# Kernel tuning notes

Hardware: AMD Instinct MI355X
Metric: run time of the kernel (lower is better)

Reference implementation:

```python
import jax, jax.numpy as jnp
import numpy as np

N_LEVELS, CPL = 4, 1024           # levels, cells per level (n_cells = 4096)
IN_D, HID, OUT_D, MLP = 512, 1024, 512, 128


def setup_inputs() -> dict:
    key = jax.random.key(0)
    ks = iter(jax.random.split(key, 32))
    r = lambda shape, s=0.05: jax.random.normal(next(ks), shape, dtype=jnp.float32) * s
    inp = {
        'x': r((1, IN_D), 1.0),
        'hiddens': r((N_LEVELS * CPL, HID), 0.1),
        'ea_W1': r((N_LEVELS, IN_D + HID, MLP)), 'ea_b1': r((N_LEVELS, MLP)),
        'ea_W2': r((N_LEVELS, MLP, OUT_D)),      'ea_b2': r((N_LEVELS, OUT_D)),
        'eg_W1': r((N_LEVELS, IN_D + HID, MLP)), 'eg_b1': r((N_LEVELS, MLP)),
        'eg_W2': r((N_LEVELS, MLP, OUT_D)),      'eg_b2': r((N_LEVELS, OUT_D)),
        'gru_Wih': r((N_LEVELS, 3 * HID, OUT_D + 1)),
        'gru_Whh': r((N_LEVELS, 3 * HID, HID)),
        'gru_bih': r((N_LEVELS, 3 * HID)), 'gru_bhh': r((N_LEVELS, 3 * HID)),
        'pred_W1': r((N_LEVELS - 1, HID, HID)), 'pred_b1': r((N_LEVELS - 1, HID)),
        'pred_W2': r((N_LEVELS - 1, HID, HID)), 'pred_b2': r((N_LEVELS - 1, HID)),
        'pei_W': r((HID * N_LEVELS, OUT_D)), 'pei_b': r((OUT_D,)),
        'step': 10,
    }
    return inp


def _forward(x, hiddens, ea_W1, ea_b1, ea_W2, ea_b2, eg_W1, eg_b1, eg_W2, eg_b2,
             gru_Wih, gru_Whh, gru_bih, gru_bhh, pred_W1, pred_b1, pred_W2, pred_b2,
             pei_W, pei_b, step):
    L = gru_Whh.shape[0]
    Hd = gru_Whh.shape[2]
    C = hiddens.shape[0] // L
    h = hiddens.reshape(L, C, Hd)                              # [L,C,H]
    xb = jnp.broadcast_to(x[0], (L, C, x.shape[-1]))           # same x for every cell
    comb = jnp.concatenate([xb, h], axis=-1)                   # [L,C,IN+H]

    def mlp(W1, b1, W2, b2):
        z = jax.nn.relu(jnp.einsum('lci,lim->lcm', comb, W1) + b1[:, None, :])
        return jnp.einsum('lcm,lmo->lco', z, W2) + b2[:, None, :]

    out = mlp(ea_W1, ea_b1, ea_W2, ea_b2) - mlp(eg_W1, eg_b1, eg_W2, eg_b2)  # a - g
    tension = jnp.mean(out ** 2, axis=-1, keepdims=True)       # [L,C,1]
    avg_tension = jnp.mean(tension)                            # mean over all cells

    # GRUCell (torch gate order r,z,n); mem input is detached in the original
    mem_in = jax.lax.stop_gradient(jnp.concatenate([out, tension], axis=-1))  # [L,C,OUT+1]
    gi = jnp.einsum('lci,lgi->lcg', mem_in, gru_Wih) + gru_bih[:, None, :]
    gh = jnp.einsum('lch,lgh->lcg', h, gru_Whh) + gru_bhh[:, None, :]
    i_r, i_z, i_n = jnp.split(gi, 3, axis=-1)
    h_r, h_z, h_n = jnp.split(gh, 3, axis=-1)
    rg = jax.nn.sigmoid(i_r + h_r)
    zg = jax.nn.sigmoid(i_z + h_z)
    ng = jnp.tanh(i_n + rg * h_n)
    new_h = jax.lax.stop_gradient((1.0 - zg) * ng + zg * h)    # self.hiddens = ...detach()

    level_means = new_h.mean(axis=1)                           # [L,H] (pre pe-update)

    # top-down predictors: predicted[lv] from level_means[lv+1]
    pz = jax.nn.relu(jnp.einsum('li,lim->lm', level_means[1:], pred_W1) + pred_b1)
    predicted = jnp.einsum('lm,lmo->lo', pz, pred_W2) + pred_b2          # [L-1,H]
    pe_signal = jax.lax.stop_gradient((predicted - level_means[:-1]) * 0.05)
    delta = jnp.zeros_like(level_means).at[:-1].add(pe_signal).at[1:].add(-0.5 * pe_signal)
    hh = new_h + delta[:, None, :]

    # per-level mean blend
    hh = 0.85 * hh + 0.15 * hh.mean(axis=1, keepdims=True)
    # faction sync: with n_factions == n_levels, factions == levels exactly
    hh = 0.85 * hh + 0.15 * hh.mean(axis=1, keepdims=True)
    if step > 5:  # debate (step is a static Python int)
        global_op = hh.mean(axis=1).mean(axis=0)               # [H]
        dc = max(1, C // 4)
        hh = hh.at[:, :dc].set(0.85 * hh[:, :dc] + 0.15 * global_op)

    combined = level_means.reshape(-1) @ pei_W + pei_b         # [OUT]
    return combined, avg_tension, hh.reshape(-1, Hd)


def reference(x, hiddens, ea_W1, ea_b1, ea_W2, ea_b2, eg_W1, eg_b1, eg_W2, eg_b2,
              gru_Wih, gru_Whh, gru_bih, gru_bhh, pred_W1, pred_b1, pred_W2, pred_b2,
              pei_W, pei_b, step):
    return _forward(x, hiddens, ea_W1, ea_b1, ea_W2, ea_b2, eg_W1, eg_b1, eg_W2, eg_b2,
                    gru_Wih, gru_Whh, gru_bih, gru_bhh, pred_W1, pred_b1, pred_W2, pred_b2,
                    pei_W, pei_b, step)
```

## Files before the change

kernel.cpp:

```cpp
#include <hip/hip_runtime.h>
#include <math.h>

#define L4   4
#define CPL  1024
#define HID  1024
#define IND  512
#define MLPD 128
#define OUTD 512
#define G3   3072
#define ROWS 4096
#define KP   544

typedef unsigned short u16;
typedef u16   u16x8  __attribute__((ext_vector_type(8)));
typedef short bf16x8 __attribute__((ext_vector_type(8)));
typedef float f32x4  __attribute__((ext_vector_type(4)));

__device__ __forceinline__ float b2f(u16 u) {
  return __uint_as_float(((unsigned int)u) << 16);
}
__device__ __forceinline__ u16 f2b(float f) {
  unsigned int x = __float_as_uint(f);
  x += 0x7fffu + ((x >> 16) & 1u);
  return (u16)(x >> 16);
}
__device__ __forceinline__ float sigm(float v) { return 1.0f/(1.0f + expf(-v)); }

struct F4 { float x, y, z, w; };
__device__ __forceinline__ F4 ld4(const void* p, size_t i, bool f32) {
  F4 r;
  if (f32) {
    float4 v = *reinterpret_cast<const float4*>((const float*)p + i);
    r.x = v.x; r.y = v.y; r.z = v.z; r.w = v.w;
  } else {
    ushort4 v = *reinterpret_cast<const ushort4*>((const u16*)p + i);
    r.x = b2f(v.x); r.y = b2f(v.y); r.z = b2f(v.z); r.w = b2f(v.w);
  }
  return r;
}
__device__ __forceinline__ float ld1(const void* p, size_t i, bool f32) {
  return f32 ? ((const float*)p)[i] : b2f(((const u16*)p)[i]);
}
__device__ __forceinline__ void st1(void* p, size_t i, float v, bool f32) {
  if (f32) ((float*)p)[i] = v; else ((u16*)p)[i] = f2b(v);
}
__device__ __forceinline__ u16x8 ldc8(const void* p, size_t i, bool f32) {
  u16x8 r;
  if (f32) {
    const float* q = (const float*)p + i;
    float4 v0 = *reinterpret_cast<const float4*>(q);
    float4 v1 = *reinterpret_cast<const float4*>(q + 4);
    r[0]=f2b(v0.x); r[1]=f2b(v0.y); r[2]=f2b(v0.z); r[3]=f2b(v0.w);
    r[4]=f2b(v1.x); r[5]=f2b(v1.y); r[6]=f2b(v1.z); r[7]=f2b(v1.w);
  } else {
    r = *reinterpret_cast<const u16x8*>((const u16*)p + i);
  }
  return r;
}

__global__ void k_detect(const void* __restrict__ x, int* __restrict__ flag) {
  int t = threadIdx.x;
  const u16* xu = (const u16*)x;
  unsigned u = xu[2*t];
  int e = (u >> 7) & 0xFF;
  int good = (e >= 96 && e <= 134) ? 1 : 0;
  __shared__ int cnt[256];
  cnt[t] = good;
  __syncthreads();
  for (int s = 128; s > 0; s >>= 1) { if (t < s) cnt[t] += cnt[t+s]; __syncthreads(); }
  if (t == 0) flag[0] = (cnt[0] < 200) ? 1 : 0;
}

__global__ void k_prep(float* __restrict__ zf, const void* __restrict__ bih,
                       const void* __restrict__ bhh, const int* __restrict__ dflag,
                       float* __restrict__ bs_r, float* __restrict__ bs_z,
                       float* __restrict__ bn_i, float* __restrict__ bn_h) {
  const bool f32 = dflag[0] != 0;
  int b = blockIdx.x, t = threadIdx.x;
  if (b < 16) {
    int idx = b*256 + t;
    int l = idx >> 10, j = idx & 1023;
    bs_r[idx] = ld1(bih, l*G3 + j, f32)        + ld1(bhh, l*G3 + j, f32);
    bs_z[idx] = ld1(bih, l*G3 + 1024 + j, f32) + ld1(bhh, l*G3 + 1024 + j, f32);
    bn_i[idx] = ld1(bih, l*G3 + 2048 + j, f32);
    bn_h[idx] = ld1(bhh, l*G3 + 2048 + j, f32);
  } else {
    int idx = (b-16)*256 + t;
    zf[idx] = 0.0f;
  }
}

__global__ void k_prep_wih(const void* __restrict__ Wih, const int* __restrict__ dflag,
                           u16* __restrict__ WihP) {
  const bool f32 = dflag[0] != 0;
  int row = blockIdx.x;
  int t = threadIdx.x;
  size_t src = (size_t)row * 513;
  size_t dst = (size_t)row * KP;
  WihP[dst + t]       = f2b(ld1(Wih, src + t, f32));
  WihP[dst + 256 + t] = f2b(ld1(Wih, src + 256 + t, f32));
  if (t < 32) {
    float v = (t == 0) ? ld1(Wih, src + 512, f32) : 0.0f;
    WihP[dst + 512 + t] = f2b(v);
  }
}

__global__ void k_prep_whh(const void* __restrict__ Whh, const int* __restrict__ dflag,
                           u16* __restrict__ WhhP) {
  const bool f32 = dflag[0] != 0;
  int t = threadIdx.x;
  int row = blockIdx.x*2 + (t >> 7);
  int c8  = (t & 127) * 8;
  size_t off = (size_t)row * HID + c8;
  u16x8 v = ldc8(Whh, off, f32);
  *reinterpret_cast<u16x8*>(&WhhP[off]) = v;
}

__global__ void k_prep_hb(const void* __restrict__ H, const int* __restrict__ dflag,
                          u16* __restrict__ HB) {
  const bool f32 = dflag[0] != 0;
  int t = threadIdx.x;
  int row = blockIdx.x*2 + (t >> 7);
  int c8  = (t & 127) * 8;
  size_t off = (size_t)row * HID + c8;
  u16x8 v = ldc8(H, off, f32);
  *reinterpret_cast<u16x8*>(&HB[off]) = v;
}

__global__ void k_prep_w1t(const void* __restrict__ eaW1, const void* __restrict__ egW1,
                           const int* __restrict__ dflag, u16* __restrict__ W1T) {
  const bool f32 = dflag[0] != 0;
  __shared__ u16 sT[128*66];
  int l = blockIdx.x, path = blockIdx.y, kt = blockIdx.z;
  int t = threadIdx.x;
  const void* W1 = path ? egW1 : eaW1;
  for (int rr = 0; rr < 64; rr += 2) {
    int r = rr + (t >> 7), m = t & 127;
    float v = ld1(W1, ((size_t)l*1536 + 512 + kt*64 + r)*MLPD + m, f32);
    sT[m*66 + r] = f2b(v);
  }
  __syncthreads();
  for (int mm = 0; mm < 128; mm += 4) {
    int m = mm + (t >> 6), kk = t & 63;
    W1T[((size_t)l*256 + path*128 + m)*1024 + kt*64 + kk] = sT[m*66 + kk];
  }
}

__global__ void k_base_acc(const void* __restrict__ x, const void* __restrict__ eaW1,
                           const void* __restrict__ egW1, const int* __restrict__ dflag,
                           float* __restrict__ baseacc) {
  const bool f32 = dflag[0] != 0;
  int l = blockIdx.x, path = blockIdx.y, kc = blockIdx.z, m = threadIdx.x;
  const void* W1 = path ? egW1 : eaW1;
  float acc = 0.0f;
  int i0 = kc*128;
  for (int i = i0; i < i0 + 128; ++i)
    acc += ld1(x, i, f32) * ld1(W1, ((size_t)l*1536 + i)*MLPD + m, f32);
  atomicAdd(&baseacc[path*512 + l*MLPD + m], acc);
}

#define LPAD 40
__global__ __launch_bounds__(256) void k_z_mfma(
    const u16* __restrict__ HB, const u16* __restrict__ W1T,
    const void* __restrict__ eab1, const void* __restrict__ egb1,
    const float* __restrict__ baseacc, const int* __restrict__ dflag,
    u16* __restrict__ Z) {
  const bool f32 = dflag[0] != 0;
  __shared__ u16 sA[2][64*LPAD];
  __shared__ u16 sB[2][64*LPAD];
  int t = threadIdx.x;
  int row0 = blockIdx.x * 64;
  int n0   = blockIdx.y * 64;
  int l    = row0 >> 10;
  int wid = t >> 6, lane = t & 63;
  int waveM = wid >> 1, waveN = wid & 1;
  int quad = lane >> 4, lcol = lane & 15;
  int arow = t >> 2, kq = (t & 3) * 8;

  f32x4 acc[2][2];
  const f32x4 zz = {0.0f,0.0f,0.0f,0.0f};
#pragma unroll
  for (int i = 0; i < 2; ++i)
#pragma unroll
    for (int j = 0; j < 2; ++j) acc[i][j] = zz;

  size_t habase = (size_t)(row0 + arow)*HID;
  const u16* Bb = W1T + ((size_t)l*256 + n0 + arow)*1024;

  u16x8 av = *reinterpret_cast<const u16x8*>(HB + habase + kq);
  u16x8 bv = *reinterpret_cast<const u16x8*>(Bb + kq);
  int cur = 0;
  for (int k0 = 0; k0 < HID; k0 += 32) {
    *reinterpret_cast<u16x8*>(&sA[cur][arow*LPAD + kq]) = av;
    *reinterpret_cast<u16x8*>(&sB[cur][arow*LPAD + kq]) = bv;
    asm volatile("s_waitcnt lgkmcnt(0)" ::: "memory");
    __builtin_amdgcn_s_barrier();
    if (k0 + 32 < HID) {
      av = *reinterpret_cast<const u16x8*>(HB + habase + k0 + 32 + kq);
      bv = *reinterpret_cast<const u16x8*>(Bb + k0 + 32 + kq);
    }
    bf16x8 af[2];
#pragma unroll
    for (int i = 0; i < 2; ++i)
      af[i] = *reinterpret_cast<const bf16x8*>(&sA[cur][(waveM*32 + i*16 + lcol)*LPAD + quad*8]);
#pragma unroll
    for (int j = 0; j < 2; ++j) {
      bf16x8 bf = *reinterpret_cast<const bf16x8*>(&sB[cur][(waveN*32 + j*16 + lcol)*LPAD + quad*8]);
#pragma unroll
      for (int i = 0; i < 2; ++i)
        acc[i][j] = __builtin_amdgcn_mfma_f32_16x16x32_bf16(af[i], bf, acc[i][j], 0, 0, 0);
    }
    cur ^= 1;
  }
#pragma unroll
  for (int j = 0; j < 2; ++j) {
    int nn = n0 + waveN*32 + j*16 + lcol;
    int path = nn >> 7, m = nn & 127;
    float bval = baseacc[path*512 + l*MLPD + m] +
                 ld1(path ? egb1 : eab1, l*MLPD + m, f32);
#pragma unroll
    for (int i = 0; i < 2; ++i)
#pragma unroll
      for (int g = 0; g < 4; ++g) {
        int r = row0 + waveM*32 + i*16 + quad*4 + g;
        float v = acc[i][j][g] + bval;
        Z[(size_t)r*256 + nn] = f2b(v > 0.0f ? v : 0.0f);
      }
  }
}

#define BM 64
#define BN 64
#define BK 16
__global__ __launch_bounds__(256) void k_out(
    const u16* __restrict__ Zb, const void* __restrict__ eaW2, const void* __restrict__ egW2,
    const void* __restrict__ eab2, const void* __restrict__ egb2,
    const int* __restrict__ dflag, u16* __restrict__ OUTT) {
  const bool f32 = dflag[0] != 0;
  __shared__ float As[BK][BM];
  __shared__ float Bs[BK][BN];
  int t = threadIdx.x;
  int row0 = blockIdx.x * BM;
  int n0   = blockIdx.y * BN;
  int l    = row0 >> 10;
  const u16* Ab = Zb + (size_t)row0 * 256;
  int tx = t & 15, ty = t >> 4;
  int am = t >> 2, akq = (t & 3) * 4;
  int bk = t >> 4, bn = (t & 15) * 4;

  float acc[4][4];
#pragma unroll
  for (int j = 0; j < 4; ++j) {
    int o = n0 + tx*4 + j;
    float bd = ld1(eab2, l*OUTD + o, f32) - ld1(egb2, l*OUTD + o, f32);
#pragma unroll
    for (int i = 0; i < 4; ++i) acc[i][j] = bd;
  }
  for (int ph = 0; ph < 2; ++ph) {
    const void* B = ph ? egW2 : eaW2;
    size_t boff = (size_t)l*MLPD*OUTD + n0;
    float sgn = ph ? -1.0f : 1.0f;
    for (int k0 = 0; k0 < MLPD; k0 += BK) {
      ushort4 avu = *reinterpret_cast<const ushort4*>(Ab + (size_t)am*256 + ph*128 + k0 + akq);
      F4 bvf = ld4(B, boff + (size_t)(k0 + bk)*OUTD + bn, f32);
      __syncthreads();
      As[akq+0][am] = b2f(avu.x); As[akq+1][am] = b2f(avu.y);
      As[akq+2][am] = b2f(avu.z); As[akq+3][am] = b2f(avu.w);
      Bs[bk][bn+0] = sgn*bvf.x; Bs[bk][bn+1] = sgn*bvf.y;
      Bs[bk][bn+2] = sgn*bvf.z; Bs[bk][bn+3] = sgn*bvf.w;
      __syncthreads();
#pragma unroll
      for (int kk = 0; kk < BK; ++kk) {
        float4 a4 = *reinterpret_cast<const float4*>(&As[kk][ty*4]);
        float4 b4 = *reinterpret_cast<const float4*>(&Bs[kk][tx*4]);
        float a[4] = {a4.x,a4.y,a4.z,a4.w};
        float b[4] = {b4.x,b4.y,b4.z,b4.w};
#pragma unroll
        for (int i = 0; i < 4; ++i)
#pragma unroll
          for (int j = 0; j < 4; ++j) acc[i][j] += a[i]*b[j];
      }
    }
  }
#pragma unroll
  for (int i = 0; i < 4; ++i) {
    int r = row0 + ty*4 + i;
#pragma unroll
    for (int j = 0; j < 4; ++j)
      OUTT[(size_t)r*KP + n0 + tx*4 + j] = f2b(acc[i][j]);
  }
}

__global__ void k_tension(u16* __restrict__ OUTT, float* __restrict__ tsum) {
  int row = blockIdx.x, t = threadIdx.x;
  u16* p = OUTT + (size_t)row*KP;
  float v0 = b2f(p[t]), v1 = b2f(p[t+256]);
  float s = v0*v0 + v1*v1;
#pragma unroll
  for (int off = 32; off > 0; off >>= 1) s += __shfl_down(s, off, 64);
  __shared__ float red[4];
  if ((t & 63) == 0) red[t >> 6] = s;
  __syncthreads();
  if (t == 0) {
    float tot = red[0] + red[1] + red[2] + red[3];
    p[512] = f2b(tot * (1.0f/512.0f));
    atomicAdd(tsum, tot);
  }
  if (t < 31) p[513 + t] = 0;
}

#define SWZ(row, ku) ((row)*64 + ((ku) ^ (((row)&7)<<3)))
__global__ __launch_bounds__(256, 2) void k_gru_mfma(
    const u16* __restrict__ OUTT, const u16* __restrict__ HB,
    const u16* __restrict__ WihP, const u16* __restrict__ WhhP,
    const void* __restrict__ H,
    const float* __restrict__ bs_r, const float* __restrict__ bs_z,
    const float* __restrict__ bn_i, const float* __restrict__ bn_h,
    const int* __restrict__ dflag, void* __restrict__ outv) {
  const bool f32 = dflag[0] != 0;
  __shared__ __align__(16) u16 sA[2][128*64];
  __shared__ __align__(16) u16 sB[2][3*64*64];
  int t = threadIdx.x;
  int bid = blockIdx.x;
  int xg = bid & 7, inner = bid >> 3;
  int l = xg & 3, jG = xg >> 2;
  int rbi = inner & 7, jbl = inner >> 3;
  int row0 = (l*8 + rbi) * 128;
  int j0   = (jG*8 + jbl) * 64;
  int wid = t >> 6, lane = t & 63;
  int waveM = wid & 1, waveJ = wid >> 1;
  int quad = lane >> 4, lcol = lane & 15;

  f32x4 acc[4][4][2];
  const f32x4 zz = {0.0f,0.0f,0.0f,0.0f};
#pragma unroll
  for (int b = 0; b < 4; ++b)
#pragma unroll
    for (int i = 0; i < 4; ++i)
#pragma unroll
      for (int j = 0; j < 2; ++j) acc[b][i][j] = zz;

  u16x8 ra[4], rbr[6];
  auto load1 = [&](int k0) {
    int kw = KP - k0;
#pragma unroll
    for (int s = 0; s < 4; ++s) {
      int idx = s*256 + t, row = idx >> 3, ch = idx & 7;
      if (ch*8 < kw)
        ra[s] = *reinterpret_cast<const u16x8*>(
            OUTT + (size_t)(row0 + row)*KP + k0 + ch*8);
      else { u16x8 z = {0,0,0,0,0,0,0,0}; ra[s] = z; }
    }
#pragma unroll
    for (int s = 0; s < 6; ++s) {
      int idx = s*256 + t, band = idx >> 9, rem = idx & 511;
      int row = rem >> 3, ch = rem & 7;
      if (ch*8 < kw)
        rbr[s] = *reinterpret_cast<const u16x8*>(
            WihP + ((size_t)l*G3 + band*1024 + j0 + row)*KP + k0 + ch*8);
      else { u16x8 z = {0,0,0,0,0,0,0,0}; rbr[s] = z; }
    }
  };
  auto load2 = [&](int k0) {
#pragma unroll
    for (int s = 0; s < 4; ++s) {
      int idx = s*256 + t, row = idx >> 3, ch = idx & 7;
      ra[s] = *reinterpret_cast<const u16x8*>(
          HB + (size_t)(row0 + row)*HID + k0 + ch*8);
    }
#pragma unroll
    for (int s = 0; s < 6; ++s) {
      int idx = s*256 + t, band = idx >> 9, rem = idx & 511;
      int row = rem >> 3, ch = rem & 7;
      rbr[s] = *reinterpret_cast<const u16x8*>(
          WhhP + ((size_t)l*G3 + band*1024 + j0 + row)*HID + k0 + ch*8);
    }
  };
  auto stage = [&](int cb) {
#pragma unroll
    for (int s = 0; s < 4; ++s) {
      int idx = s*256 + t, row = idx >> 3, ch = idx & 7;
      *reinterpret_cast<u16x8*>(&sA[cb][SWZ(row, ch*8)]) = ra[s];
    }
#pragma unroll
    for (int s = 0; s < 6; ++s) {
      int idx = s*256 + t, band = idx >> 9, rem = idx & 511;
      int row = rem >> 3, ch = rem & 7;
      *reinterpret_cast<u16x8*>(&sB[cb][band*4096 + SWZ(row, ch*8)]) = rbr[s];
    }
  };

  int cur = 0;
  load1(0);
  for (int k0 = 0; k0 < KP; k0 += 64) {
    stage(cur);
    asm volatile("s_waitcnt lgkmcnt(0)" ::: "memory");
    __builtin_amdgcn_s_barrier();
    if (k0 + 64 < KP) load1(k0 + 64);
    else              load2(0);
    __builtin_amdgcn_s_setprio(1);
#pragma unroll
    for (int kc = 0; kc < 2; ++kc) {
      bf16x8 af[4];
#pragma unroll
      for (int i = 0; i < 4; ++i) {
        int rl = waveM*64 + i*16 + lcol;
        af[i] = *reinterpret_cast<const bf16x8*>(&sA[cur][SWZ(rl, kc*32 + quad*8)]);
      }
#pragma unroll
      for (int b = 0; b < 3; ++b)
#pragma unroll
        for (int jj = 0; jj < 2; ++jj) {
          int jl = waveJ*32 + jj*16 + lcol;
          bf16x8 bf = *reinterpret_cast<const bf16x8*>(
              &sB[cur][b*4096 + SWZ(jl, kc*32 + quad*8)]);
#pragma unroll
          for (int i = 0; i < 4; ++i)
            acc[b][i][jj] = __builtin_amdgcn_mfma_f32_16x16x32_bf16(
                af[i], bf, acc[b][i][jj], 0, 0, 0);
        }
    }
    __builtin_amdgcn_s_setprio(0);
    cur ^= 1;
  }
  for (int k0 = 0; k0 < HID; k0 += 64) {
    stage(cur);
    asm volatile("s_waitcnt lgkmcnt(0)" ::: "memory");
    __builtin_amdgcn_s_barrier();
    if (k0 + 64 < HID) load2(k0 + 64);
    __builtin_amdgcn_s_setprio(1);
#pragma unroll
    for (int kc = 0; kc < 2; ++kc) {
      bf16x8 af[4];
#pragma unroll
      for (int i = 0; i < 4; ++i) {
        int rl = waveM*64 + i*16 + lcol;
        af[i] = *reinterpret_cast<const bf16x8*>(&sA[cur][SWZ(rl, kc*32 + quad*8)]);
      }
#pragma unroll
      for (int b = 0; b < 3; ++b) {
        int ai = (b < 2) ? b : 3;
#pragma unroll
        for (int jj = 0; jj < 2; ++jj) {
          int jl = waveJ*32 + jj*16 + lcol;
          bf16x8 bf = *reinterpret_cast<const bf16x8*>(
              &sB[cur][b*4096 + SWZ(jl, kc*32 + quad*8)]);
#pragma unroll
          for (int i = 0; i < 4; ++i)
            acc[ai][i][jj] = __builtin_amdgcn_mfma_f32_16x16x32_bf16(
                af[i], bf, acc[ai][i][jj], 0, 0, 0);
        }
      }
    }
    __builtin_amdgcn_s_setprio(0);
    cur ^= 1;
  }
#pragma unroll
  for (int i = 0; i < 4; ++i)
#pragma unroll
    for (int jj = 0; jj < 2; ++jj) {
      int j = j0 + waveJ*32 + jj*16 + lcol;
      float br = bs_r[l*HID + j], bz = bs_z[l*HID + j];
      float bi = bn_i[l*HID + j], bh = bn_h[l*HID + j];
#pragma unroll
      for (int g = 0; g < 4; ++g) {
        int r = row0 + waveM*64 + i*16 + quad*4 + g;
        float rg = sigm(acc[0][i][jj][g] + br);
        float zg = sigm(acc[1][i][jj][g] + bz);
        float ng = tanhf(acc[2][i][jj][g] + bi + rg*(acc[3][i][jj][g] + bh));
        float hv = ld1(H, (size_t)r*HID + j, f32);
        st1(outv, 513 + (size_t)r*HID + j, (1.0f - zg)*ng + zg*hv, f32);
      }
    }
}

__global__ void k_lm_acc(const void* __restrict__ outv, const int* __restrict__ dflag,
                         float* __restrict__ lm) {
  const bool f32 = dflag[0] != 0;
  int l = blockIdx.x, cc = blockIdx.y, t = threadIdx.x;
  float s0=0.f, s1=0.f, s2=0.f, s3=0.f;
  for (int c = cc*16; c < cc*16 + 16; ++c) {
    size_t base = 513 + (size_t)(l*CPL + c)*HID;
    s0 += ld1(outv, base + t,       f32);
    s1 += ld1(outv, base + 256 + t, f32);
    s2 += ld1(outv, base + 512 + t, f32);
    s3 += ld1(outv, base + 768 + t, f32);
  }
  atomicAdd(&lm[l*HID + t],       s0);
  atomicAdd(&lm[l*HID + 256 + t], s1);
  atomicAdd(&lm[l*HID + 512 + t], s2);
  atomicAdd(&lm[l*HID + 768 + t], s3);
}
__global__ void k_lmfin(float* __restrict__ lm) {
  int idx = blockIdx.x*256 + threadIdx.x;
  lm[idx] *= (1.0f/1024.0f);
}

__global__ void k_pz_acc(const float* __restrict__ lm, const void* __restrict__ pW1,
                         const int* __restrict__ dflag, float* __restrict__ pz) {
  const bool f32 = dflag[0] != 0;
  int lv = blockIdx.x, mb = blockIdx.y, kc = blockIdx.z;
  int m = mb*256 + threadIdx.x;
  float acc = 0.0f;
  int i0 = kc*32;
  const float* lmp = lm + (lv + 1)*HID;
  for (int i = i0; i < i0 + 32; ++i)
    acc += lmp[i] * ld1(pW1, ((size_t)lv*HID + i)*HID + m, f32);
  atomicAdd(&pz[lv*HID + m], acc);
}
__global__ void k_pzfin(float* __restrict__ pz, const void* __restrict__ pb1,
                        const int* __restrict__ dflag) {
  const bool f32 = dflag[0] != 0;
  int idx = blockIdx.x*256 + threadIdx.x;
  float v = pz[idx] + ld1(pb1, idx, f32);
  pz[idx] = v > 0.0f ? v : 0.0f;
}
__global__ void k_pe_acc(const float* __restrict__ pz, const void* __restrict__ pW2,
                         const int* __restrict__ dflag, float* __restrict__ pe) {
  const bool f32 = dflag[0] != 0;
  int lv = blockIdx.x, ob = blockIdx.y, kc = blockIdx.z;
  int o = ob*256 + threadIdx.x;
  float acc = 0.0f;
  int m0 = kc*32;
  const float* pzp = pz + lv*HID;
  for (int m = m0; m < m0 + 32; ++m)
    acc += pzp[m] * ld1(pW2, ((size_t)lv*HID + m)*HID + o, f32);
  atomicAdd(&pe[lv*HID + o], acc);
}
__global__ void k_pefin(float* __restrict__ pe, const void* __restrict__ pb2,
                        const float* __restrict__ lm, const int* __restrict__ dflag) {
  const bool f32 = dflag[0] != 0;
  int idx = blockIdx.x*256 + threadIdx.x;
  pe[idx] = (pe[idx] + ld1(pb2, idx, f32) - lm[idx]) * 0.05f;
}

__global__ void k_addc_gop(const float* __restrict__ lm, const float* __restrict__ pe,
                           float* __restrict__ addc, float* __restrict__ gop) {
  int j = blockIdx.x*256 + threadIdx.x;
  float pe0 = pe[j], pe1 = pe[1024 + j], pe2 = pe[2048 + j];
  float d0 = pe0, d1 = pe1 - 0.5f*pe0, d2 = pe2 - 0.5f*pe1, d3 = -0.5f*pe2;
  float l0 = lm[j], l1 = lm[1024 + j], l2 = lm[2048 + j], l3 = lm[3072 + j];
  addc[j]        = 0.2775f*l0 + d0;
  addc[1024 + j] = 0.2775f*l1 + d1;
  addc[2048 + j] = 0.2775f*l2 + d2;
  addc[3072 + j] = 0.2775f*l3 + d3;
  gop[j] = 0.25f*((l0 + d0) + (l1 + d1) + (l2 + d2) + (l3 + d3));
}

__global__ void k_comb_acc(const float* __restrict__ lm, const void* __restrict__ peiW,
                           const int* __restrict__ dflag, float* __restrict__ comb) {
  const bool f32 = dflag[0] != 0;
  int ob = blockIdx.x, kc = blockIdx.y;
  int o = ob*256 + threadIdx.x;
  float acc = 0.0f;
  int i0 = kc*128;
  for (int i = i0; i < i0 + 128; ++i)
    acc += lm[i] * ld1(peiW, (size_t)i*OUTD + o, f32);
  atomicAdd(&comb[o], acc);
}
__global__ void k_fin(const float* __restrict__ comb, const void* __restrict__ peib,
                      const float* __restrict__ tsum, const int* __restrict__ dflag,
                      void* __restrict__ outv) {
  const bool f32 = dflag[0] != 0;
  int o = blockIdx.x*256 + threadIdx.x;
  st1(outv, o, comb[o] + ld1(peib, o, f32), f32);
  if (o == 0) st1(outv, 512, tsum[0] * (1.0f/(4096.0f*512.0f)), f32);
}

__global__ void k_hh(void* __restrict__ outv, const float* __restrict__ addc,
                     const float* __restrict__ gop, const int* __restrict__ step,
                     const int* __restrict__ dflag) {
  const bool f32 = dflag[0] != 0;
  int row = blockIdx.x, t = threadIdx.x;
  int l = row >> 10, c = row & 1023;
  bool debate = (step[0] > 5) && (c < 256);
  size_t base = 513 + (size_t)row*HID;
#pragma unroll
  for (int k = 0; k < 4; ++k) {
    int j = t + k*256;
    float v = 0.7225f * ld1(outv, base + j, f32) + addc[l*HID + j];
    if (debate) v = 0.85f*v + 0.15f*gop[j];
    st1(outv, base + j, v, f32);
  }
}

extern "C" void kernel_launch(void* const* d_in, const int* in_sizes, int n_in,
                              void* d_out, int out_size, void* d_ws, size_t ws_size,
                              hipStream_t stream) {
  (void)in_sizes; (void)n_in; (void)out_size; (void)ws_size;
  const void* x    = d_in[0];
  const void* hid  = d_in[1];
  const void* eaW1 = d_in[2];
  const void* eab1 = d_in[3];
  const void* eaW2 = d_in[4];
  const void* eab2 = d_in[5];
  const void* egW1 = d_in[6];
  const void* egb1 = d_in[7];
  const void* egW2 = d_in[8];
  const void* egb2 = d_in[9];
  const void* gWih = d_in[10];
  const void* gWhh = d_in[11];
  const void* gbih = d_in[12];
  const void* gbhh = d_in[13];
  const void* pW1  = d_in[14];
  const void* pb1  = d_in[15];
  const void* pW2  = d_in[16];
  const void* pb2  = d_in[17];
  const void* peiW = d_in[18];
  const void* peib = d_in[19];
  const int*  step = (const int*)d_in[20];

  float* wsf = (float*)d_ws;
  float* tsum    = wsf + 0;
  float* baseacc = wsf + 64;
  float* lm      = wsf + 1088;
  float* pz      = wsf + 5184;
  float* pe      = wsf + 8256;
  float* comb    = wsf + 11328;
  int*   dflag   = (int*)(wsf + 12288);
  float* bs_r    = wsf + 12352;
  float* bs_z    = wsf + 16448;
  float* bn_i    = wsf + 20544;
  float* bn_h    = wsf + 24640;
  float* addc    = wsf + 28736;
  float* gop     = wsf + 32832;
  u16* Zb   = (u16*)(wsf + 33856);
  u16* OUTT = Zb + (size_t)4096*256;
  u16* WihP = OUTT + (size_t)4096*KP;
  u16* HB   = WihP + (size_t)12288*KP;
  u16* WhhP = HB   + (size_t)4096*1024;
  u16* W1T  = OUTT;

  k_detect   <<<dim3(1),        dim3(256), 0, stream>>>(x, dflag);
  k_prep     <<<dim3(64),       dim3(256), 0, stream>>>(wsf, gbih, gbhh, dflag,
                                                        bs_r, bs_z, bn_i, bn_h);
  k_prep_wih <<<dim3(12288),    dim3(256), 0, stream>>>(gWih, dflag, WihP);
  k_prep_whh <<<dim3(6144),     dim3(256), 0, stream>>>(gWhh, dflag, WhhP);
  k_prep_hb  <<<dim3(2048),     dim3(256), 0, stream>>>(hid, dflag, HB);
  k_prep_w1t <<<dim3(4,2,16),   dim3(256), 0, stream>>>(eaW1, egW1, dflag, W1T);
  k_base_acc <<<dim3(4,2,4),    dim3(128), 0, stream>>>(x, eaW1, egW1, dflag, baseacc);
  k_z_mfma   <<<dim3(64,4),     dim3(256), 0, stream>>>(HB, W1T, eab1, egb1,
                                                        baseacc, dflag, Zb);
  k_out      <<<dim3(64,8),     dim3(256), 0, stream>>>(Zb, eaW2, egW2, eab2, egb2,
                                                        dflag, OUTT);
  k_tension  <<<dim3(4096),     dim3(256), 0, stream>>>(OUTT, tsum);
  k_gru_mfma <<<dim3(512),      dim3(256), 0, stream>>>(OUTT, HB, WihP, WhhP, hid,
                                                        bs_r, bs_z, bn_i, bn_h,
                                                        dflag, d_out);
  k_lm_acc   <<<dim3(4,64),     dim3(256), 0, stream>>>(d_out, dflag, lm);
  k_lmfin    <<<dim3(16),       dim3(256), 0, stream>>>(lm);
  k_pz_acc   <<<dim3(3,4,32),   dim3(256), 0, stream>>>(lm, pW1, dflag, pz);
  k_pzfin    <<<dim3(12),       dim3(256), 0, stream>>>(pz, pb1, dflag);
  k_pe_acc   <<<dim3(3,4,32),   dim3(256), 0, stream>>>(pz, pW2, dflag, pe);
  k_pefin    <<<dim3(12),       dim3(256), 0, stream>>>(pe, pb2, lm, dflag);
  k_addc_gop <<<dim3(4),        dim3(256), 0, stream>>>(lm, pe, addc, gop);
  k_comb_acc <<<dim3(2,32),     dim3(256), 0, stream>>>(lm, peiW, dflag, comb);
  k_fin      <<<dim3(2),        dim3(256), 0, stream>>>(comb, peib, tsum, dflag, d_out);
  k_hh       <<<dim3(4096),     dim3(256), 0, stream>>>(d_out, addc, gop, step, dflag);
}
```

Before: 448.6 us.

## Use MFMA for second MLP layer, widen z-GEMM K tile, fuse level-mean into GRU

The scalar FP32 second-layer GEMM is replaced by a bf16 MFMA kernel. It reads a new prepacked, sign-folded W2 matrix, so the ea and eg paths become one K=256 GEMM. The first-layer MFMA kernel now uses a 64-wide K tile with swizzled LDS and priority hints. The per-level mean reduction moves into the GRU epilogue through an LDS reduction and atomics, which removes a separate pass over the output. In exchange it adds a prep kernel, and it lowers W2 precision to bf16.

```diff
diff --git a/kernel.cpp b/kernel.cpp
--- a/kernel.cpp
+++ b/kernel.cpp
@@ -27,17 +27,6 @@
 __device__ __forceinline__ float sigm(float v) { return 1.0f/(1.0f + expf(-v)); }
 
 struct F4 { float x, y, z, w; };
-__device__ __forceinline__ F4 ld4(const void* p, size_t i, bool f32) {
-  F4 r;
-  if (f32) {
-    float4 v = *reinterpret_cast<const float4*>((const float*)p + i);
-    r.x = v.x; r.y = v.y; r.z = v.z; r.w = v.w;
-  } else {
-    ushort4 v = *reinterpret_cast<const ushort4*>((const u16*)p + i);
-    r.x = b2f(v.x); r.y = b2f(v.y); r.z = b2f(v.z); r.w = b2f(v.w);
-  }
-  return r;
-}
 __device__ __forceinline__ float ld1(const void* p, size_t i, bool f32) {
   return f32 ? ((const float*)p)[i] : b2f(((const u16*)p)[i]);
 }
@@ -146,6 +135,26 @@
   }
 }
 
+__global__ void k_prep_w2m(const void* __restrict__ eaW2, const void* __restrict__ egW2,
+                           const int* __restrict__ dflag, u16* __restrict__ W2M) {
+  const bool f32 = dflag[0] != 0;
+  __shared__ u16 sT[128*130];
+  int l = blockIdx.x, path = blockIdx.y, ot = blockIdx.z;
+  int t = threadIdx.x;
+  const void* W2 = path ? egW2 : eaW2;
+  float sgn = path ? -1.0f : 1.0f;
+  for (int rr = 0; rr < 128; rr += 2) {
+    int r = rr + (t >> 7), o = t & 127;
+    float v = ld1(W2, ((size_t)l*MLPD + r)*OUTD + ot*128 + o, f32);
+    sT[o*130 + r] = f2b(sgn*v);
+  }
+  __syncthreads();
+  for (int oo = 0; oo < 128; oo += 2) {
+    int o = oo + (t >> 7), m = t & 127;
+    W2M[((size_t)l*OUTD + ot*128 + o)*256 + path*128 + m] = sT[o*130 + m];
+  }
+}
+
 __global__ void k_base_acc(const void* __restrict__ x, const void* __restrict__ eaW1,
                            const void* __restrict__ egW1, const int* __restrict__ dflag,
                            float* __restrict__ baseacc) {
@@ -159,15 +168,16 @@
   atomicAdd(&baseacc[path*512 + l*MLPD + m], acc);
 }
 
-#define LPAD 40
+#define SWZ(row, ku) ((row)*64 + ((ku) ^ (((row)&7)<<3)))
+
 __global__ __launch_bounds__(256) void k_z_mfma(
     const u16* __restrict__ HB, const u16* __restrict__ W1T,
     const void* __restrict__ eab1, const void* __restrict__ egb1,
     const float* __restrict__ baseacc, const int* __restrict__ dflag,
     u16* __restrict__ Z) {
   const bool f32 = dflag[0] != 0;
-  __shared__ u16 sA[2][64*LPAD];
-  __shared__ u16 sB[2][64*LPAD];
+  __shared__ __align__(16) u16 sA[2][64*64];
+  __shared__ __align__(16) u16 sB[2][64*64];
   int t = threadIdx.x;
   int row0 = blockIdx.x * 64;
   int n0   = blockIdx.y * 64;
@@ -175,7 +185,6 @@
   int wid = t >> 6, lane = t & 63;
   int waveM = wid >> 1, waveN = wid & 1;
   int quad = lane >> 4, lcol = lane & 15;
-  int arow = t >> 2, kq = (t & 3) * 8;
 
   f32x4 acc[2][2];
   const f32x4 zz = {0.0f,0.0f,0.0f,0.0f};
@@ -184,32 +193,52 @@
 #pragma unroll
     for (int j = 0; j < 2; ++j) acc[i][j] = zz;
 
-  size_t habase = (size_t)(row0 + arow)*HID;
-  const u16* Bb = W1T + ((size_t)l*256 + n0 + arow)*1024;
-
-  u16x8 av = *reinterpret_cast<const u16x8*>(HB + habase + kq);
-  u16x8 bv = *reinterpret_cast<const u16x8*>(Bb + kq);
+  u16x8 ra[2], rb[2];
+  auto loadk = [&](int k0) {
+#pragma unroll
+    for (int s = 0; s < 2; ++s) {
+      int idx = s*256 + t, row = idx >> 3, ch = idx & 7;
+      ra[s] = *reinterpret_cast<const u16x8*>(
+          HB + (size_t)(row0 + row)*HID + k0 + ch*8);
+      rb[s] = *reinterpret_cast<const u16x8*>(
+          W1T + ((size_t)l*256 + n0 + row)*1024 + k0 + ch*8);
+    }
+  };
+  auto stage = [&](int cb) {
+#pragma unroll
+    for (int s = 0; s < 2; ++s) {
+      int idx = s*256 + t, row = idx >> 3, ch = idx & 7;
+      *reinterpret_cast<u16x8*>(&sA[cb][SWZ(row, ch*8)]) = ra[s];
+      *reinterpret_cast<u16x8*>(&sB[cb][SWZ(row, ch*8)]) = rb[s];
+    }
+  };
+
   int cur = 0;
-  for (int k0 = 0; k0 < HID; k0 += 32) {
-    *reinterpret_cast<u16x8*>(&sA[cur][arow*LPAD + kq]) = av;
-    *reinterpret_cast<u16x8*>(&sB[cur][arow*LPAD + kq]) = bv;
+  loadk(0);
+  for (int k0 = 0; k0 < HID; k0 += 64) {
+    stage(cur);
     asm volatile("s_waitcnt lgkmcnt(0)" ::: "memory");
     __builtin_amdgcn_s_barrier();
-    if (k0 + 32 < HID) {
-      av = *reinterpret_cast<const u16x8*>(HB + habase + k0 + 32 + kq);
-      bv = *reinterpret_cast<const u16x8*>(Bb + k0 + 32 + kq);
-    }
-    bf16x8 af[2];
-#pragma unroll
-    for (int i = 0; i < 2; ++i)
-      af[i] = *reinterpret_cast<const bf16x8*>(&sA[cur][(waveM*32 + i*16 + lcol)*LPAD + quad*8]);
-#pragma unroll
-    for (int j = 0; j < 2; ++j) {
-      bf16x8 bf = *reinterpret_cast<const bf16x8*>(&sB[cur][(waveN*32 + j*16 + lcol)*LPAD + quad*8]);
-#pragma unroll
-      for (int i = 0; i < 2; ++i)
-        acc[i][j] = __builtin_amdgcn_mfma_f32_16x16x32_bf16(af[i], bf, acc[i][j], 0, 0, 0);
-    }
+    if (k0 + 64 < HID) loadk(k0 + 64);
+    __builtin_amdgcn_s_setprio(1);
+#pragma unroll
+    for (int kc = 0; kc < 2; ++kc) {
+      bf16x8 af[2];
+#pragma unroll
+      for (int i = 0; i < 2; ++i) {
+        int rl = waveM*32 + i*16 + lcol;
+        af[i] = *reinterpret_cast<const bf16x8*>(&sA[cur][SWZ(rl, kc*32 + quad*8)]);
+      }
+#pragma unroll
+      for (int j = 0; j < 2; ++j) {
+        int jl = waveN*32 + j*16 + lcol;
+        bf16x8 bf = *reinterpret_cast<const bf16x8*>(&sB[cur][SWZ(jl, kc*32 + quad*8)]);
+#pragma unroll
+        for (int i = 0; i < 2; ++i)
+          acc[i][j] = __builtin_amdgcn_mfma_f32_16x16x32_bf16(af[i], bf, acc[i][j], 0, 0, 0);
+      }
+    }
+    __builtin_amdgcn_s_setprio(0);
     cur ^= 1;
   }
 #pragma unroll
@@ -229,65 +258,95 @@
   }
 }
 
-#define BM 64
-#define BN 64
-#define BK 16
-__global__ __launch_bounds__(256) void k_out(
-    const u16* __restrict__ Zb, const void* __restrict__ eaW2, const void* __restrict__ egW2,
+__global__ __launch_bounds__(256) void k_outm(
+    const u16* __restrict__ Zb, const u16* __restrict__ W2M,
     const void* __restrict__ eab2, const void* __restrict__ egb2,
     const int* __restrict__ dflag, u16* __restrict__ OUTT) {
   const bool f32 = dflag[0] != 0;
-  __shared__ float As[BK][BM];
-  __shared__ float Bs[BK][BN];
-  int t = threadIdx.x;
-  int row0 = blockIdx.x * BM;
-  int n0   = blockIdx.y * BN;
+  __shared__ __align__(16) u16 sA[2][128*64];
+  __shared__ __align__(16) u16 sB[2][64*64];
+  int t = threadIdx.x;
+  int row0 = blockIdx.x * 128;
+  int n0   = blockIdx.y * 64;
   int l    = row0 >> 10;
-  const u16* Ab = Zb + (size_t)row0 * 256;
-  int tx = t & 15, ty = t >> 4;
-  int am = t >> 2, akq = (t & 3) * 4;
-  int bk = t >> 4, bn = (t & 15) * 4;
-
-  float acc[4][4];
-#pragma unroll
-  for (int j = 0; j < 4; ++j) {
-    int o = n0 + tx*4 + j;
+  int wid = t >> 6, lane = t & 63;
+  int waveM = wid & 1, waveJ = wid >> 1;
+  int quad = lane >> 4, lcol = lane & 15;
+
+  f32x4 acc[4][2];
+  const f32x4 zz = {0.0f,0.0f,0.0f,0.0f};
+#pragma unroll
+  for (int i = 0; i < 4; ++i)
+#pragma unroll
+    for (int j = 0; j < 2; ++j) acc[i][j] = zz;
+
+  u16x8 ra[4], rb[2];
+  auto loadk = [&](int k0) {
+#pragma unroll
+    for (int s = 0; s < 4; ++s) {
+      int idx = s*256 + t, row = idx >> 3, ch = idx & 7;
+      ra[s] = *reinterpret_cast<const u16x8*>(
+          Zb + (size_t)(row0 + row)*256 + k0 + ch*8);
+    }
+#pragma unroll
+    for (int s = 0; s < 2; ++s) {
+      int idx = s*256 + t, row = idx >> 3, ch = idx & 7;
+      rb[s] = *reinterpret_cast<const u16x8*>(
+          W2M + ((size_t)l*OUTD + n0 + row)*256 + k0 + ch*8);
+    }
+  };
+  auto stage = [&](int cb) {
+#pragma unroll
+    for (int s = 0; s < 4; ++s) {
+      int idx = s*256 + t, row = idx >> 3, ch = idx & 7;
+      *reinterpret_cast<u16x8*>(&sA[cb][SWZ(row, ch*8)]) = ra[s];
+    }
+#pragma unroll
+    for (int s = 0; s < 2; ++s) {
+      int idx = s*256 + t, row = idx >> 3, ch = idx & 7;
+      *reinterpret_cast<u16x8*>(&sB[cb][SWZ(row, ch*8)]) = rb[s];
+    }
+  };
+
+  int cur = 0;
+  loadk(0);
+  for (int k0 = 0; k0 < 256; k0 += 64) {
+    stage(cur);
+    asm volatile("s_waitcnt lgkmcnt(0)" ::: "memory");
+    __builtin_amdgcn_s_barrier();
+    if (k0 + 64 < 256) loadk(k0 + 64);
+    __builtin_amdgcn_s_setprio(1);
+#pragma unroll
+    for (int kc = 0; kc < 2; ++kc) {
+      bf16x8 af[4];
+#pragma unroll
+      for (int i = 0; i < 4; ++i) {
+        int rl = waveM*64 + i*16 + lcol;
+        af[i] = *reinterpret_cast<const bf16x8*>(&sA[cur][SWZ(rl, kc*32 + quad*8)]);
+      }
+#pragma unroll
+      for (int jj = 0; jj < 2; ++jj) {
+        int jl = waveJ*32 + jj*16 + lcol;
+        bf16x8 bf = *reinterpret_cast<const bf16x8*>(&sB[cur][SWZ(jl, kc*32 + quad*8)]);
+#pragma unroll
+        for (int i = 0; i < 4; ++i)
+          acc[i][jj] = __builtin_amdgcn_mfma_f32_16x16x32_bf16(af[i], bf, acc[i][jj], 0, 0, 0);
+      }
+    }
+    __builtin_amdgcn_s_setprio(0);
+    cur ^= 1;
+  }
+#pragma unroll
+  for (int jj = 0; jj < 2; ++jj) {
+    int o = n0 + waveJ*32 + jj*16 + lcol;
     float bd = ld1(eab2, l*OUTD + o, f32) - ld1(egb2, l*OUTD + o, f32);
 #pragma unroll
-    for (int i = 0; i < 4; ++i) acc[i][j] = bd;
-  }
-  for (int ph = 0; ph < 2; ++ph) {
-    const void* B = ph ? egW2 : eaW2;
-    size_t boff = (size_t)l*MLPD*OUTD + n0;
-    float sgn = ph ? -1.0f : 1.0f;
-    for (int k0 = 0; k0 < MLPD; k0 += BK) {
-      ushort4 avu = *reinterpret_cast<const ushort4*>(Ab + (size_t)am*256 + ph*128 + k0 + akq);
-      F4 bvf = ld4(B, boff + (size_t)(k0 + bk)*OUTD + bn, f32);
-      __syncthreads();
-      As[akq+0][am] = b2f(avu.x); As[akq+1][am] = b2f(avu.y);
-      As[akq+2][am] = b2f(avu.z); As[akq+3][am] = b2f(avu.w);
-      Bs[bk][bn+0] = sgn*bvf.x; Bs[bk][bn+1] = sgn*bvf.y;
-      Bs[bk][bn+2] = sgn*bvf.z; Bs[bk][bn+3] = sgn*bvf.w;
-      __syncthreads();
-#pragma unroll
-      for (int kk = 0; kk < BK; ++kk) {
-        float4 a4 = *reinterpret_cast<const float4*>(&As[kk][ty*4]);
-        float4 b4 = *reinterpret_cast<const float4*>(&Bs[kk][tx*4]);
-        float a[4] = {a4.x,a4.y,a4.z,a4.w};
-        float b[4] = {b4.x,b4.y,b4.z,b4.w};
-#pragma unroll
-        for (int i = 0; i < 4; ++i)
-#pragma unroll
-          for (int j = 0; j < 4; ++j) acc[i][j] += a[i]*b[j];
-      }
-    }
-  }
-#pragma unroll
-  for (int i = 0; i < 4; ++i) {
-    int r = row0 + ty*4 + i;
-#pragma unroll
-    for (int j = 0; j < 4; ++j)
-      OUTT[(size_t)r*KP + n0 + tx*4 + j] = f2b(acc[i][j]);
+    for (int i = 0; i < 4; ++i)
+#pragma unroll
+      for (int g = 0; g < 4; ++g) {
+        int r = row0 + waveM*64 + i*16 + quad*4 + g;
+        OUTT[(size_t)r*KP + o] = f2b(acc[i][jj][g] + bd);
+      }
   }
 }
 
@@ -309,14 +368,14 @@
   if (t < 31) p[513 + t] = 0;
 }
 
-#define SWZ(row, ku) ((row)*64 + ((ku) ^ (((row)&7)<<3)))
 __global__ __launch_bounds__(256, 2) void k_gru_mfma(
     const u16* __restrict__ OUTT, const u16* __restrict__ HB,
     const u16* __restrict__ WihP, const u16* __restrict__ WhhP,
     const void* __restrict__ H,
     const float* __restrict__ bs_r, const float* __restrict__ bs_z,
     const float* __restrict__ bn_i, const float* __restrict__ bn_h,
-    const int* __restrict__ dflag, void* __restrict__ outv) {
+    const int* __restrict__ dflag, void* __restrict__ outv,
+    float* __restrict__ lm) {
   const bool f32 = dflag[0] != 0;
   __shared__ __align__(16) u16 sA[2][128*64];
   __shared__ __align__(16) u16 sB[2][3*64*64];
@@ -455,6 +514,7 @@
     __builtin_amdgcn_s_setprio(0);
     cur ^= 1;
   }
+  float psum[2] = {0.0f, 0.0f};
 #pragma unroll
   for (int i = 0; i < 4; ++i)
 #pragma unroll
@@ -469,28 +529,28 @@
         float zg = sigm(acc[1][i][jj][g] + bz);
         float ng = tanhf(acc[2][i][jj][g] + bi + rg*(acc[3][i][jj][g] + bh));
         float hv = ld1(H, (size_t)r*HID + j, f32);
-        st1(outv, 513 + (size_t)r*HID + j, (1.0f - zg)*ng + zg*hv, f32);
-      }
-    }
-}
-
-__global__ void k_lm_acc(const void* __restrict__ outv, const int* __restrict__ dflag,
-                         float* __restrict__ lm) {
-  const bool f32 = dflag[0] != 0;
-  int l = blockIdx.x, cc = blockIdx.y, t = threadIdx.x;
-  float s0=0.f, s1=0.f, s2=0.f, s3=0.f;
-  for (int c = cc*16; c < cc*16 + 16; ++c) {
-    size_t base = 513 + (size_t)(l*CPL + c)*HID;
-    s0 += ld1(outv, base + t,       f32);
-    s1 += ld1(outv, base + 256 + t, f32);
-    s2 += ld1(outv, base + 512 + t, f32);
-    s3 += ld1(outv, base + 768 + t, f32);
-  }
-  atomicAdd(&lm[l*HID + t],       s0);
-  atomicAdd(&lm[l*HID + 256 + t], s1);
-  atomicAdd(&lm[l*HID + 512 + t], s2);
-  atomicAdd(&lm[l*HID + 768 + t], s3);
-}
+        float nh = (1.0f - zg)*ng + zg*hv;
+        st1(outv, 513 + (size_t)r*HID + j, nh, f32);
+        psum[jj] += nh;
+      }
+    }
+  __syncthreads();
+  float* red = reinterpret_cast<float*>(&sA[0][0]);
+  int slot = waveM*4 + quad;
+#pragma unroll
+  for (int jj = 0; jj < 2; ++jj) {
+    int jl = waveJ*32 + jj*16 + lcol;
+    red[jl*8 + slot] = psum[jj];
+  }
+  __syncthreads();
+  if (t < 64) {
+    float s = 0.0f;
+#pragma unroll
+    for (int k = 0; k < 8; ++k) s += red[t*8 + k];
+    atomicAdd(&lm[l*HID + j0 + t], s);
+  }
+}
+
 __global__ void k_lmfin(float* __restrict__ lm) {
   int idx = blockIdx.x*256 + threadIdx.x;
   lm[idx] *= (1.0f/1024.0f);
@@ -629,6 +689,7 @@
   u16* WihP = OUTT + (size_t)4096*KP;
   u16* HB   = WihP + (size_t)12288*KP;
   u16* WhhP = HB   + (size_t)4096*1024;
+  u16* W2M  = WhhP + (size_t)12288*1024;
   u16* W1T  = OUTT;
 
   k_detect   <<<dim3(1),        dim3(256), 0, stream>>>(x, dflag);
@@ -638,16 +699,16 @@
   k_prep_whh <<<dim3(6144),     dim3(256), 0, stream>>>(gWhh, dflag, WhhP);
   k_prep_hb  <<<dim3(2048),     dim3(256), 0, stream>>>(hid, dflag, HB);
   k_prep_w1t <<<dim3(4,2,16),   dim3(256), 0, stream>>>(eaW1, egW1, dflag, W1T);
+  k_prep_w2m <<<dim3(4,2,4),    dim3(256), 0, stream>>>(eaW2, egW2, dflag, W2M);
   k_base_acc <<<dim3(4,2,4),    dim3(128), 0, stream>>>(x, eaW1, egW1, dflag, baseacc);
   k_z_mfma   <<<dim3(64,4),     dim3(256), 0, stream>>>(HB, W1T, eab1, egb1,
                                                         baseacc, dflag, Zb);
-  k_out      <<<dim3(64,8),     dim3(256), 0, stream>>>(Zb, eaW2, egW2, eab2, egb2,
+  k_outm     <<<dim3(32,8),     dim3(256), 0, stream>>>(Zb, W2M, eab2, egb2,
                                                         dflag, OUTT);
   k_tension  <<<dim3(4096),     dim3(256), 0, stream>>>(OUTT, tsum);
   k_gru_mfma <<<dim3(512),      dim3(256), 0, stream>>>(OUTT, HB, WihP, WhhP, hid,
                                                         bs_r, bs_z, bn_i, bn_h,
-                                                        dflag, d_out);
-  k_lm_acc   <<<dim3(4,64),     dim3(256), 0, stream>>>(d_out, dflag, lm);
+                                                        dflag, d_out, lm);
   k_lmfin    <<<dim3(16),       dim3(256), 0, stream>>>(lm);
   k_pz_acc   <<<dim3(3,4,32),   dim3(256), 0, stream>>>(lm, pW1, dflag, pz);
   k_pzfin    <<<dim3(12),       dim3(256), 0, stream>>>(pz, pb1, dflag);
```

Result: no change. 452.8 us (+0.9%).
